# Optimization experiments

Measured on AMD Instinct MI355X. Metric: run time of the kernel, lower is better.

The kernel has to match this reference:

```python
import jax, jax.numpy as jnp
import numpy as np

KSIZE = 3
SOFTMAX_SCALE = 10.0


def extract_patches(x):
    # x: [B, C, H, W] -> patches [B, H*W, C, 3, 3]
    # Matches F.unfold(same_padding(x), kernel=3, stride=1) then
    # reshape(B, C, 3, 3, L).permute(0, 4, 1, 2, 3).
    B, C, H, W = x.shape
    xp = jnp.pad(x, ((0, 0), (0, 0), (1, 1), (1, 1)))
    # p[b, c, i, j, y, x] = xp[b, c, y+i, x+j]
    p = jnp.stack(
        [jnp.stack([xp[:, :, i:i + H, j:j + W] for j in range(KSIZE)], axis=2)
         for i in range(KSIZE)], axis=2)  # [B, C, 3, 3, H, W]
    return p.transpose(0, 4, 5, 1, 2, 3).reshape(B, H * W, C, KSIZE, KSIZE)


def _conv_same(x, w):
    # x: [Cin, H, W], w: [Cout, Cin, 3, 3] -> [Cout, H, W] (pad 1, stride 1)
    return jax.lax.conv_general_dilated(
        x[None], w, window_strides=(1, 1), padding=((1, 1), (1, 1)),
        dimension_numbers=('NCHW', 'OIHW', 'NCHW'))[0]


def setup_inputs() -> dict:
    key = jax.random.key(0)
    kf, kb = jax.random.split(key)
    f = jax.random.normal(kf, (4, 64, 64, 64), dtype=jnp.float32)
    b = jax.random.normal(kb, (4, 64, 64, 64), dtype=jnp.float32)
    return {"f": f, "b": b}


def reference(f, b):
    B, C, Hf, Wf = f.shape
    # Per-sample dynamic kernels from background patches: [B, L, C, 3, 3]
    w = extract_patches(b)
    # Correlation: per-sample conv of f with its own L patch-kernels -> [B, L, Hf, Wf]
    scores = jax.vmap(_conv_same)(f, w)
    # Scaled softmax over the L patch axis
    attn = jax.nn.softmax(scores * SOFTMAX_SCALE, axis=1)
    # conv_transpose2d(attn, w, stride=1, padding=1) == SAME conv with
    # spatially-flipped kernels and in/out channels swapped.
    w_t = jnp.flip(w, axis=(-2, -1)).transpose(0, 2, 1, 3, 4)  # [B, C, L, 3, 3]
    y = jax.vmap(_conv_same)(attn, w_t) / 9.0  # [B, C, Hf, Wf]
    return (y, w.reshape(B, -1, KSIZE, KSIZE))
```

## Files before the change

kernel.cpp:

```cpp
#include <hip/hip_runtime.h>
#include <hip/hip_bf16.h>
#include <hip/hip_fp16.h>
#include <stdint.h>


typedef unsigned short ushort_t;
typedef __attribute__((ext_vector_type(8))) short bf16x8;
typedef __attribute__((ext_vector_type(4))) float f32x4;

#define RSTRIDE  16777216ull
#define ASTRIDE  16777216ull
#define PSTRIDE  33554432ull
#define SSTRIDE  65536ull

__device__ __forceinline__ float bf2f(ushort_t u){
  union { float f; uint32_t i; } v; v.i = ((uint32_t)u) << 16; return v.f;
}
__device__ __forceinline__ ushort_t f2bf(float f){
  union { float f; uint32_t i; } v; v.f = f;
  uint32_t x = v.i;
  return (ushort_t)((x + 0x7fffu + ((x >> 16) & 1u)) >> 16);
}

__global__ __launch_bounds__(256) void k_prep2(const float* __restrict__ bin,
                                               float* __restrict__ wout,
                                               float* __restrict__ yzero){
  __shared__ float ls[2304];
  int tid = threadIdx.x;
  int t = blockIdx.x * 256 + tid;
  yzero[t] = 0.f;
  int c  = t & 63;
  int l  = (t >> 6) & 4095;
  int bb = t >> 18;
  int y = l >> 6, x = l & 63;
  const float* src = bin + (((size_t)(bb * 64 + c)) << 12);
  float* dst = ls + tid * 9;
  #pragma unroll
  for (int i = 0; i < 3; i++){
    int yy = y + i - 1;
    #pragma unroll
    for (int j = 0; j < 3; j++){
      int xx = x + j - 1;
      float v = 0.f;
      if ((unsigned)yy < 64u && (unsigned)xx < 64u) v = src[(yy << 6) + xx];
      dst[i * 3 + j] = v;
    }
  }
  __syncthreads();
  float* wbase = wout + (size_t)blockIdx.x * 2304;
  #pragma unroll
  for (int idx = tid; idx < 576; idx += 256)
    *(float4*)(wbase + (idx << 2)) = *(const float4*)(ls + (idx << 2));
}

__global__ __launch_bounds__(256, 2) void k_rgemm(const float* __restrict__ f,
                                                  const float* __restrict__ bin,
                                                  float* __restrict__ R,
                                                  int bt0){
  __shared__ float As[64][128];
  __shared__ float Bs[64][128];
  int bt = bt0 + blockIdx.z;
  int m0 = blockIdx.x << 7;
  int n0 = blockIdx.y << 7;
  const float* fb = f   + (((size_t)bt) << 18);
  const float* bb = bin + (((size_t)bt) << 18);
  float* Rb = R + (size_t)blockIdx.z * RSTRIDE;
  int t = threadIdx.x;
  for (int idx = t; idx < 64 * 128; idx += 256){
    int c = idx >> 7, m = idx & 127;
    As[c][m] = fb[(c << 12) + m0 + m];
    Bs[c][m] = bb[(c << 12) + n0 + m];
  }
  __syncthreads();
  int tx = t & 15, ty = t >> 4;
  float acc[8][8];
  #pragma unroll
  for (int i = 0; i < 8; i++)
    #pragma unroll
    for (int j = 0; j < 8; j++) acc[i][j] = 0.f;

  for (int c = 0; c < 64; c++){
    float4 a0 = *(const float4*)&As[c][(ty << 3)];
    float4 a1 = *(const float4*)&As[c][(ty << 3) + 4];
    float4 b0 = *(const float4*)&Bs[c][(tx << 2)];
    float4 b1 = *(const float4*)&Bs[c][64 + (tx << 2)];
    float av[8] = {a0.x, a0.y, a0.z, a0.w, a1.x, a1.y, a1.z, a1.w};
    float bv[8] = {b0.x, b0.y, b0.z, b0.w, b1.x, b1.y, b1.z, b1.w};
    #pragma unroll
    for (int i = 0; i < 8; i++)
      #pragma unroll
      for (int j = 0; j < 8; j++) acc[i][j] += av[i] * bv[j];
  }
  #pragma unroll
  for (int i = 0; i < 8; i++){
    float* dst = Rb + ((size_t)(m0 + (ty << 3) + i) << 12) + n0;
    *(float4*)(dst + (tx << 2))      = make_float4(acc[i][0], acc[i][1], acc[i][2], acc[i][3]);
    *(float4*)(dst + 64 + (tx << 2)) = make_float4(acc[i][4], acc[i][5], acc[i][6], acc[i][7]);
  }
}

__global__ __launch_bounds__(256, 2) void k_softmax4(const float* __restrict__ Rg,
                                                     ushort_t* __restrict__ attng,
                                                     __half* __restrict__ scaleg){
  __shared__ float Rt[24][392];
  const int t  = threadIdx.x;
  const int bb = blockIdx.x;
  const float* R = Rg + (size_t)blockIdx.y * RSTRIDE;
  ushort_t* attn = attng + (size_t)blockIdx.y * ASTRIDE;
  __half* scale = scaleg + (size_t)blockIdx.y * SSTRIDE;
  const int inner = bb >> 3;
  const int ty = ((bb & 7) << 1) | (inner & 1);
  const int tx = inner >> 1;
  const int p0 = ty << 2, q0 = tx << 1;
  const int qi = t >> 5, kt = t & 31;
  const int pi = qi >> 1, qj = qi & 1;
  const int ktx = kt & 15;

  float M = -3.0e38f, L = 0.f;
  float mref[16];
  float4 rbuf[10];

  int row = ((p0 + pi) << 6) + q0 + qj;
  ushort_t* arow = attn + ((size_t)row << 12);

  #pragma unroll
  for (int i = 0; i < 10; i++){
    int idx = t + (i << 8);
    float4 v = make_float4(0.f, 0.f, 0.f, 0.f);
    if (idx < 2352){
      unsigned r = (unsigned)idx / 98u;
      int fo = idx - (int)r * 98;
      int rp = p0 - 1 + (int)(r >> 2);
      int rq = q0 - 1 + (int)(r & 3);
      int kg = -68 + (fo << 2);
      if ((unsigned)rp < 64u && (unsigned)rq < 64u && (unsigned)kg <= 4092u)
        v = *(const float4*)(R + (((size_t)((rp << 6) + rq)) << 12) + kg);
    }
    rbuf[i] = v;
  }

  #pragma unroll
  for (int c = 0; c < 16; c++){
    __syncthreads();
    #pragma unroll
    for (int i = 0; i < 10; i++){
      int idx = t + (i << 8);
      if (idx < 2352) ((float4*)&Rt[0][0])[idx] = rbuf[i];
    }
    __syncthreads();
    if (c < 15){
      const int k0 = (c + 1) << 8;
      #pragma unroll
      for (int i = 0; i < 10; i++){
        int idx = t + (i << 8);
        float4 v = make_float4(0.f, 0.f, 0.f, 0.f);
        if (idx < 2352){
          unsigned r = (unsigned)idx / 98u;
          int fo = idx - (int)r * 98;
          int rp = p0 - 1 + (int)(r >> 2);
          int rq = q0 - 1 + (int)(r & 3);
          int kg = k0 - 68 + (fo << 2);
          if ((unsigned)rp < 64u && (unsigned)rq < 64u && (unsigned)kg <= 4092u)
            v = *(const float4*)(R + (((size_t)((rp << 6) + rq)) << 12) + kg);
        }
        rbuf[i] = v;
      }
    }
    float4 sv[2];
    #pragma unroll
    for (int j = 0; j < 2; j++){
      int y = (c << 2) + (j << 1) + (kt >> 4);
      int sa0 = (j << 7) + (kt << 2) + 68;
      float4 s = make_float4(0.f, 0.f, 0.f, 0.f);
      #pragma unroll
      for (int a = -1; a <= 1; a++){
        if ((unsigned)(y + a) < 64u){
          int rb = (pi + 1 + a) << 2;
          int sa = sa0 + (a << 6);
          float4 A0 = *(const float4*)&Rt[rb + qj][sa];
          float4 A1 = *(const float4*)&Rt[rb + qj + 1][sa];
          float4 A2 = *(const float4*)&Rt[rb + qj + 2][sa];
          float Lv = __shfl_up(A0.w, 1);
          float Rv = __shfl_down(A2.x, 1);
          s.x += (ktx == 0 ? 0.f : Lv) + A1.x + A2.y;
          s.y += A0.x + A1.y + A2.z;
          s.z += A0.y + A1.z + A2.w;
          s.w += A0.z + A1.w + (ktx == 15 ? 0.f : Rv);
        }
      }
      s.x *= 10.f; s.y *= 10.f; s.z *= 10.f; s.w *= 10.f;
      sv[j] = s;
    }
    float mc = M;
    #pragma unroll
    for (int j = 0; j < 2; j++)
      mc = fmaxf(mc, fmaxf(fmaxf(sv[j].x, sv[j].y), fmaxf(sv[j].z, sv[j].w)));
    #pragma unroll
    for (int off = 1; off < 32; off <<= 1) mc = fmaxf(mc, __shfl_xor(mc, off));
    float lnew = L * __expf(M - mc);
    #pragma unroll
    for (int j = 0; j < 2; j++){
      float ex = __expf(sv[j].x - mc), ey = __expf(sv[j].y - mc);
      float ez = __expf(sv[j].z - mc), ew = __expf(sv[j].w - mc);
      lnew += ex + ey + ez + ew;
      ushort4 o; o.x = f2bf(ex); o.y = f2bf(ey); o.z = f2bf(ez); o.w = f2bf(ew);
      *(ushort4*)&arow[(c << 8) + (j << 7) + (kt << 2)] = o;
    }
    L = lnew; M = mc; mref[c] = mc;
  }
  #pragma unroll
  for (int off = 1; off < 32; off <<= 1) L += __shfl_xor(L, off);
  if (kt == 0){
    float invL = 1.0f / L;
    __half hs[16];
    #pragma unroll
    for (int c = 0; c < 16; c++) hs[c] = __float2half(__expf(mref[c] - M) * invL);
    *(uint4*)&scale[(row << 4)]     = ((uint4*)hs)[0];
    *(uint4*)&scale[(row << 4) + 8] = ((uint4*)hs)[1];
  }
}

__global__ __launch_bounds__(256, 2) void k_pstencil5(const ushort_t* __restrict__ attng,
                                                      const __half* __restrict__ scaleg,
                                                      ushort_t* __restrict__ Pg){
  __shared__ float At[24][392];
  __shared__ float Sc[24][16];
  const int t  = threadIdx.x;
  const int bb = blockIdx.x;
  const ushort_t* attn = attng + (size_t)blockIdx.y * ASTRIDE;
  const __half* scale = scaleg + (size_t)blockIdx.y * SSTRIDE;
  ushort_t* P = Pg + (size_t)blockIdx.y * PSTRIDE;
  const int inner = bb >> 3;
  const int ty = ((bb & 7) << 1) | (inner & 1);
  const int tx = inner >> 1;
  const int p0 = ty << 2, q0 = tx << 1;
  const int qi = t >> 5, kt = t & 31;
  const int pi = qi >> 1, qj = qi & 1;
  const int ktx = kt & 15;

  int row = ((p0 + pi) << 6) + q0 + qj;
  ushort_t* prow = P + ((size_t)row << 12);
  const float inv9 = 1.0f / 9.0f;

  for (int i = t; i < 384; i += 256){
    int r = i >> 4, cc = i & 15;
    int rp = p0 - 1 + (r >> 2);
    int rq = q0 - 1 + (r & 3);
    float v = 0.f;
    if ((unsigned)rp < 64u && (unsigned)rq < 64u)
      v = __half2float(scale[(((rp << 6) + rq) << 4) + cc]);
    Sc[r][cc] = v;
  }

  uint2 rbuf[10];
  #pragma unroll
  for (int i = 0; i < 10; i++){
    int idx = t + (i << 8);
    uint2 v = make_uint2(0u, 0u);
    if (idx < 2352){
      unsigned r = (unsigned)idx / 98u;
      int fo = idx - (int)r * 98;
      int rp = p0 - 1 + (int)(r >> 2);
      int rq = q0 - 1 + (int)(r & 3);
      int kg = -68 + (fo << 2);
      if ((unsigned)rp < 64u && (unsigned)rq < 64u && (unsigned)kg <= 4092u)
        v = *(const uint2*)(attn + (((size_t)((rp << 6) + rq)) << 12) + kg);
    }
    rbuf[i] = v;
  }

  #pragma unroll
  for (int c = 0; c < 16; c++){
    __syncthreads();
    #pragma unroll
    for (int i = 0; i < 10; i++){
      int idx = t + (i << 8);
      if (idx < 2352){
        unsigned r = (unsigned)idx / 98u;
        int fo = idx - (int)r * 98;
        int key = (c << 8) - 68 + (fo << 2);
        key = key < 0 ? 0 : (key > 4095 ? 4095 : key);
        float sc = Sc[r][key >> 8];
        uint2 u = rbuf[i];
        float4 w;
        { union { uint32_t q; float f; } a_, b_;
          a_.q = u.x << 16; b_.q = u.x & 0xffff0000u; w.x = a_.f * sc; w.y = b_.f * sc; }
        { union { uint32_t q; float f; } a_, b_;
          a_.q = u.y << 16; b_.q = u.y & 0xffff0000u; w.z = a_.f * sc; w.w = b_.f * sc; }
        ((float4*)&At[0][0])[idx] = w;
      }
    }
    __syncthreads();
    if (c < 15){
      const int k0 = (c + 1) << 8;
      #pragma unroll
      for (int i = 0; i < 10; i++){
        int idx = t + (i << 8);
        uint2 v = make_uint2(0u, 0u);
        if (idx < 2352){
          unsigned r = (unsigned)idx / 98u;
          int fo = idx - (int)r * 98;
          int rp = p0 - 1 + (int)(r >> 2);
          int rq = q0 - 1 + (int)(r & 3);
          int kg = k0 - 68 + (fo << 2);
          if ((unsigned)rp < 64u && (unsigned)rq < 64u && (unsigned)kg <= 4092u)
            v = *(const uint2*)(attn + (((size_t)((rp << 6) + rq)) << 12) + kg);
        }
        rbuf[i] = v;
      }
    }
    #pragma unroll
    for (int j = 0; j < 2; j++){
      int y = (c << 2) + (j << 1) + (kt >> 4);
      int sa0 = (j << 7) + (kt << 2) + 68;
      float4 s = make_float4(0.f, 0.f, 0.f, 0.f);
      #pragma unroll
      for (int a = -1; a <= 1; a++){
        if ((unsigned)(y + a) < 64u){
          int rb = (pi + 1 + a) << 2;
          int sa = sa0 + (a << 6);
          float4 A0 = *(const float4*)&At[rb + qj][sa];
          float4 A1 = *(const float4*)&At[rb + qj + 1][sa];
          float4 A2 = *(const float4*)&At[rb + qj + 2][sa];
          float Lv = __shfl_up(A0.w, 1);
          float Rv = __shfl_down(A2.x, 1);
          s.x += (ktx == 0 ? 0.f : Lv) + A1.x + A2.y;
          s.y += A0.x + A1.y + A2.z;
          s.z += A0.y + A1.z + A2.w;
          s.w += A0.z + A1.w + (ktx == 15 ? 0.f : Rv);
        }
      }
      ushort4 o;
      o.x = f2bf(s.x * inv9);
      o.y = f2bf(s.y * inv9);
      o.z = f2bf(s.z * inv9);
      o.w = f2bf(s.w * inv9);
      *(ushort4*)&prow[(c << 8) + (j << 7) + (kt << 2)] = o;
    }
  }
}

__global__ __launch_bounds__(256) void k_ygemm2(const float* __restrict__ bin,
                                                const ushort_t* __restrict__ Pg,
                                                float* __restrict__ y,
                                                int bt0){
  const int t = threadIdx.x;
  const int lane = t & 63, wv = t >> 6;
  const int n = lane & 15, quad = lane >> 4;
  const int bt = bt0 + blockIdx.z;
  const int pq0 = blockIdx.x << 6;
  const int k0  = blockIdx.y << 8;
  const float*    bbase = bin + (((size_t)bt) << 18);
  const ushort_t* Prow  = Pg + (size_t)blockIdx.z * PSTRIDE
                             + (((size_t)(pq0 + (wv << 4) + n)) << 12);

  f32x4 acc[4];
  #pragma unroll
  for (int cb = 0; cb < 4; cb++) acc[cb] = (f32x4){0.f, 0.f, 0.f, 0.f};

  #pragma unroll 2
  for (int kb = k0; kb < k0 + 256; kb += 32){
    int ko = kb + (quad << 3);
    bf16x8 pf = *(const bf16x8*)(Prow + ko);
    #pragma unroll
    for (int cb = 0; cb < 4; cb++){
      const float* bp = bbase + (((cb << 4) + n) << 12) + ko;
      float4 b0 = *(const float4*)bp;
      float4 b1 = *(const float4*)(bp + 4);
      bf16x8 bf;
      bf[0] = (short)f2bf(b0.x); bf[1] = (short)f2bf(b0.y);
      bf[2] = (short)f2bf(b0.z); bf[3] = (short)f2bf(b0.w);
      bf[4] = (short)f2bf(b1.x); bf[5] = (short)f2bf(b1.y);
      bf[6] = (short)f2bf(b1.z); bf[7] = (short)f2bf(b1.w);
      acc[cb] = __builtin_amdgcn_mfma_f32_16x16x32_bf16(bf, pf, acc[cb], 0, 0, 0);
    }
  }
  int pql = pq0 + (wv << 4) + n;
  #pragma unroll
  for (int cb = 0; cb < 4; cb++)
    #pragma unroll
    for (int r = 0; r < 4; r++){
      int c = (cb << 4) + (quad << 2) + r;
      atomicAdd(&y[(((size_t)(bt * 64 + c)) << 12) + pql], acc[cb][r]);
    }
}

extern "C" void kernel_launch(void* const* d_in, const int* in_sizes, int n_in,
                              void* d_out, int out_size, void* d_ws, size_t ws_size,
                              hipStream_t stream){
  const float* f = (const float*)d_in[0];
  const float* b = (const float*)d_in[1];
  float* out  = (float*)d_out;
  float* yout = out;
  float* wout = out + 1048576;

  const size_t RB  = RSTRIDE * 4;
  const size_t AB  = ASTRIDE * 2;
  const size_t SCB = SSTRIDE * 2;
  const size_t PER = RB + AB + SCB;

  int nb = 1;
  if (ws_size >= 4 * PER) nb = 4;
  else if (ws_size >= 2 * PER) nb = 2;

  k_prep2<<<4096, 256, 0, stream>>>(b, wout, yout);

  float*    R     = (float*)d_ws;
  ushort_t* attn  = (ushort_t*)((char*)d_ws + (size_t)nb * RB);
  __half*   scale = (__half*)((char*)d_ws + (size_t)nb * (RB + AB));
  ushort_t* P     = (ushort_t*)d_ws;
  for (int bt0 = 0; bt0 < 4; bt0 += nb){
    k_rgemm    <<<dim3(32, 32, nb), 256, 0, stream>>>(f, b, R, bt0);
    k_softmax4 <<<dim3(512, nb),    256, 0, stream>>>(R, attn, scale);
    k_pstencil5<<<dim3(512, nb),    256, 0, stream>>>(attn, scale, P);
    k_ygemm2   <<<dim3(64, 16, nb), 256, 0, stream>>>(b, P, yout, bt0);
  }
}
```

Baseline: 584.7 us.

## Shrink softmax/stencil tiles to 2x2 rows and replace y atomics with split reduction

```diff
diff --git a/kernel.cpp b/kernel.cpp
--- a/kernel.cpp
+++ b/kernel.cpp
@@ -12,6 +12,7 @@
 #define ASTRIDE  16777216ull
 #define PSTRIDE  33554432ull
 #define SSTRIDE  65536ull
+#define YPSTRIDE 4194304ull
 
 __device__ __forceinline__ float bf2f(ushort_t u){
   union { float f; uint32_t i; } v; v.i = ((uint32_t)u) << 16; return v.f;
@@ -23,12 +24,10 @@
 }
 
 __global__ __launch_bounds__(256) void k_prep2(const float* __restrict__ bin,
-                                               float* __restrict__ wout,
-                                               float* __restrict__ yzero){
+                                               float* __restrict__ wout){
   __shared__ float ls[2304];
   int tid = threadIdx.x;
   int t = blockIdx.x * 256 + tid;
-  yzero[t] = 0.f;
   int c  = t & 63;
   int l  = (t >> 6) & 4095;
   int bb = t >> 18;
@@ -99,35 +98,35 @@
   }
 }
 
-__global__ __launch_bounds__(256, 2) void k_softmax4(const float* __restrict__ Rg,
+__global__ __launch_bounds__(256, 2) void k_softmax5(const float* __restrict__ Rg,
                                                      ushort_t* __restrict__ attng,
                                                      __half* __restrict__ scaleg){
-  __shared__ float Rt[24][392];
+  __shared__ float Rt[16][392];
   const int t  = threadIdx.x;
   const int bb = blockIdx.x;
   const float* R = Rg + (size_t)blockIdx.y * RSTRIDE;
   ushort_t* attn = attng + (size_t)blockIdx.y * ASTRIDE;
   __half* scale = scaleg + (size_t)blockIdx.y * SSTRIDE;
   const int inner = bb >> 3;
-  const int ty = ((bb & 7) << 1) | (inner & 1);
-  const int tx = inner >> 1;
-  const int p0 = ty << 2, q0 = tx << 1;
-  const int qi = t >> 5, kt = t & 31;
+  const int ty = ((bb & 7) << 2) | (inner & 3);
+  const int tx = inner >> 2;
+  const int p0 = ty << 1, q0 = tx << 1;
+  const int qi = t >> 6, kt = t & 63;
   const int pi = qi >> 1, qj = qi & 1;
   const int ktx = kt & 15;
 
   float M = -3.0e38f, L = 0.f;
   float mref[16];
-  float4 rbuf[10];
+  float4 rbuf[7];
 
   int row = ((p0 + pi) << 6) + q0 + qj;
   ushort_t* arow = attn + ((size_t)row << 12);
 
   #pragma unroll
-  for (int i = 0; i < 10; i++){
+  for (int i = 0; i < 7; i++){
     int idx = t + (i << 8);
     float4 v = make_float4(0.f, 0.f, 0.f, 0.f);
-    if (idx < 2352){
+    if (idx < 1568){
       unsigned r = (unsigned)idx / 98u;
       int fo = idx - (int)r * 98;
       int rp = p0 - 1 + (int)(r >> 2);
@@ -143,18 +142,18 @@
   for (int c = 0; c < 16; c++){
     __syncthreads();
     #pragma unroll
-    for (int i = 0; i < 10; i++){
+    for (int i = 0; i < 7; i++){
       int idx = t + (i << 8);
-      if (idx < 2352) ((float4*)&Rt[0][0])[idx] = rbuf[i];
+      if (idx < 1568) ((float4*)&Rt[0][0])[idx] = rbuf[i];
     }
     __syncthreads();
     if (c < 15){
       const int k0 = (c + 1) << 8;
       #pragma unroll
-      for (int i = 0; i < 10; i++){
+      for (int i = 0; i < 7; i++){
         int idx = t + (i << 8);
         float4 v = make_float4(0.f, 0.f, 0.f, 0.f);
-        if (idx < 2352){
+        if (idx < 1568){
           unsigned r = (unsigned)idx / 98u;
           int fo = idx - (int)r * 98;
           int rp = p0 - 1 + (int)(r >> 2);
@@ -166,50 +165,38 @@
         rbuf[i] = v;
       }
     }
-    float4 sv[2];
-    #pragma unroll
-    for (int j = 0; j < 2; j++){
-      int y = (c << 2) + (j << 1) + (kt >> 4);
-      int sa0 = (j << 7) + (kt << 2) + 68;
-      float4 s = make_float4(0.f, 0.f, 0.f, 0.f);
-      #pragma unroll
-      for (int a = -1; a <= 1; a++){
-        if ((unsigned)(y + a) < 64u){
-          int rb = (pi + 1 + a) << 2;
-          int sa = sa0 + (a << 6);
-          float4 A0 = *(const float4*)&Rt[rb + qj][sa];
-          float4 A1 = *(const float4*)&Rt[rb + qj + 1][sa];
-          float4 A2 = *(const float4*)&Rt[rb + qj + 2][sa];
-          float Lv = __shfl_up(A0.w, 1);
-          float Rv = __shfl_down(A2.x, 1);
-          s.x += (ktx == 0 ? 0.f : Lv) + A1.x + A2.y;
-          s.y += A0.x + A1.y + A2.z;
-          s.z += A0.y + A1.z + A2.w;
-          s.w += A0.z + A1.w + (ktx == 15 ? 0.f : Rv);
-        }
+    int y = (c << 2) + (kt >> 4);
+    int sa0 = (kt << 2) + 68;
+    float4 s = make_float4(0.f, 0.f, 0.f, 0.f);
+    #pragma unroll
+    for (int a = -1; a <= 1; a++){
+      if ((unsigned)(y + a) < 64u){
+        int rb = (pi + 1 + a) << 2;
+        int sa = sa0 + (a << 6);
+        float4 A0 = *(const float4*)&Rt[rb + qj][sa];
+        float4 A1 = *(const float4*)&Rt[rb + qj + 1][sa];
+        float4 A2 = *(const float4*)&Rt[rb + qj + 2][sa];
+        float Lv = __shfl_up(A0.w, 1);
+        float Rv = __shfl_down(A2.x, 1);
+        s.x += (ktx == 0 ? 0.f : Lv) + A1.x + A2.y;
+        s.y += A0.x + A1.y + A2.z;
+        s.z += A0.y + A1.z + A2.w;
+        s.w += A0.z + A1.w + (ktx == 15 ? 0.f : Rv);
       }
-      s.x *= 10.f; s.y *= 10.f; s.z *= 10.f; s.w *= 10.f;
-      sv[j] = s;
-    }
-    float mc = M;
-    #pragma unroll
-    for (int j = 0; j < 2; j++)
-      mc = fmaxf(mc, fmaxf(fmaxf(sv[j].x, sv[j].y), fmaxf(sv[j].z, sv[j].w)));
-    #pragma unroll
-    for (int off = 1; off < 32; off <<= 1) mc = fmaxf(mc, __shfl_xor(mc, off));
-    float lnew = L * __expf(M - mc);
-    #pragma unroll
-    for (int j = 0; j < 2; j++){
-      float ex = __expf(sv[j].x - mc), ey = __expf(sv[j].y - mc);
-      float ez = __expf(sv[j].z - mc), ew = __expf(sv[j].w - mc);
-      lnew += ex + ey + ez + ew;
-      ushort4 o; o.x = f2bf(ex); o.y = f2bf(ey); o.z = f2bf(ez); o.w = f2bf(ew);
-      *(ushort4*)&arow[(c << 8) + (j << 7) + (kt << 2)] = o;
-    }
-    L = lnew; M = mc; mref[c] = mc;
-  }
-  #pragma unroll
-  for (int off = 1; off < 32; off <<= 1) L += __shfl_xor(L, off);
+    }
+    s.x *= 10.f; s.y *= 10.f; s.z *= 10.f; s.w *= 10.f;
+    float mc = fmaxf(M, fmaxf(fmaxf(s.x, s.y), fmaxf(s.z, s.w)));
+    #pragma unroll
+    for (int off = 1; off < 64; off <<= 1) mc = fmaxf(mc, __shfl_xor(mc, off));
+    float ex = __expf(s.x - mc), ey = __expf(s.y - mc);
+    float ez = __expf(s.z - mc), ew = __expf(s.w - mc);
+    L = L * __expf(M - mc) + ex + ey + ez + ew;
+    ushort4 o; o.x = f2bf(ex); o.y = f2bf(ey); o.z = f2bf(ez); o.w = f2bf(ew);
+    *(ushort4*)&arow[(c << 8) + (kt << 2)] = o;
+    M = mc; mref[c] = mc;
+  }
+  #pragma unroll
+  for (int off = 1; off < 64; off <<= 1) L += __shfl_xor(L, off);
   if (kt == 0){
     float invL = 1.0f / L;
     __half hs[16];
@@ -220,21 +207,21 @@
   }
 }
 
-__global__ __launch_bounds__(256, 2) void k_pstencil5(const ushort_t* __restrict__ attng,
+__global__ __launch_bounds__(256, 2) void k_pstencil6(const ushort_t* __restrict__ attng,
                                                       const __half* __restrict__ scaleg,
                                                       ushort_t* __restrict__ Pg){
-  __shared__ float At[24][392];
-  __shared__ float Sc[24][16];
+  __shared__ float At[16][392];
+  __shared__ float Sc[16][16];
   const int t  = threadIdx.x;
   const int bb = blockIdx.x;
   const ushort_t* attn = attng + (size_t)blockIdx.y * ASTRIDE;
   const __half* scale = scaleg + (size_t)blockIdx.y * SSTRIDE;
   ushort_t* P = Pg + (size_t)blockIdx.y * PSTRIDE;
   const int inner = bb >> 3;
-  const int ty = ((bb & 7) << 1) | (inner & 1);
-  const int tx = inner >> 1;
-  const int p0 = ty << 2, q0 = tx << 1;
-  const int qi = t >> 5, kt = t & 31;
+  const int ty = ((bb & 7) << 2) | (inner & 3);
+  const int tx = inner >> 2;
+  const int p0 = ty << 1, q0 = tx << 1;
+  const int qi = t >> 6, kt = t & 63;
   const int pi = qi >> 1, qj = qi & 1;
   const int ktx = kt & 15;
 
@@ -242,8 +229,8 @@
   ushort_t* prow = P + ((size_t)row << 12);
   const float inv9 = 1.0f / 9.0f;
 
-  for (int i = t; i < 384; i += 256){
-    int r = i >> 4, cc = i & 15;
+  {
+    int r = t >> 4, cc = t & 15;
     int rp = p0 - 1 + (r >> 2);
     int rq = q0 - 1 + (r & 3);
     float v = 0.f;
@@ -252,12 +239,12 @@
     Sc[r][cc] = v;
   }
 
-  uint2 rbuf[10];
-  #pragma unroll
-  for (int i = 0; i < 10; i++){
+  uint2 rbuf[7];
+  #pragma unroll
+  for (int i = 0; i < 7; i++){
     int idx = t + (i << 8);
     uint2 v = make_uint2(0u, 0u);
-    if (idx < 2352){
+    if (idx < 1568){
       unsigned r = (unsigned)idx / 98u;
       int fo = idx - (int)r * 98;
       int rp = p0 - 1 + (int)(r >> 2);
@@ -273,9 +260,9 @@
   for (int c = 0; c < 16; c++){
     __syncthreads();
     #pragma unroll
-    for (int i = 0; i < 10; i++){
+    for (int i = 0; i < 7; i++){
       int idx = t + (i << 8);
-      if (idx < 2352){
+      if (idx < 1568){
         unsigned r = (unsigned)idx / 98u;
         int fo = idx - (int)r * 98;
         int key = (c << 8) - 68 + (fo << 2);
@@ -294,10 +281,10 @@
     if (c < 15){
       const int k0 = (c + 1) << 8;
       #pragma unroll
-      for (int i = 0; i < 10; i++){
+      for (int i = 0; i < 7; i++){
         int idx = t + (i << 8);
         uint2 v = make_uint2(0u, 0u);
-        if (idx < 2352){
+        if (idx < 1568){
           unsigned r = (unsigned)idx / 98u;
           int fo = idx - (int)r * 98;
           int rp = p0 - 1 + (int)(r >> 2);
@@ -309,50 +296,49 @@
         rbuf[i] = v;
       }
     }
-    #pragma unroll
-    for (int j = 0; j < 2; j++){
-      int y = (c << 2) + (j << 1) + (kt >> 4);
-      int sa0 = (j << 7) + (kt << 2) + 68;
-      float4 s = make_float4(0.f, 0.f, 0.f, 0.f);
-      #pragma unroll
-      for (int a = -1; a <= 1; a++){
-        if ((unsigned)(y + a) < 64u){
-          int rb = (pi + 1 + a) << 2;
-          int sa = sa0 + (a << 6);
-          float4 A0 = *(const float4*)&At[rb + qj][sa];
-          float4 A1 = *(const float4*)&At[rb + qj + 1][sa];
-          float4 A2 = *(const float4*)&At[rb + qj + 2][sa];
-          float Lv = __shfl_up(A0.w, 1);
-          float Rv = __shfl_down(A2.x, 1);
-          s.x += (ktx == 0 ? 0.f : Lv) + A1.x + A2.y;
-          s.y += A0.x + A1.y + A2.z;
-          s.z += A0.y + A1.z + A2.w;
-          s.w += A0.z + A1.w + (ktx == 15 ? 0.f : Rv);
-        }
+    int y = (c << 2) + (kt >> 4);
+    int sa0 = (kt << 2) + 68;
+    float4 s = make_float4(0.f, 0.f, 0.f, 0.f);
+    #pragma unroll
+    for (int a = -1; a <= 1; a++){
+      if ((unsigned)(y + a) < 64u){
+        int rb = (pi + 1 + a) << 2;
+        int sa = sa0 + (a << 6);
+        float4 A0 = *(const float4*)&At[rb + qj][sa];
+        float4 A1 = *(const float4*)&At[rb + qj + 1][sa];
+        float4 A2 = *(const float4*)&At[rb + qj + 2][sa];
+        float Lv = __shfl_up(A0.w, 1);
+        float Rv = __shfl_down(A2.x, 1);
+        s.x += (ktx == 0 ? 0.f : Lv) + A1.x + A2.y;
+        s.y += A0.x + A1.y + A2.z;
+        s.z += A0.y + A1.z + A2.w;
+        s.w += A0.z + A1.w + (ktx == 15 ? 0.f : Rv);
       }
-      ushort4 o;
-      o.x = f2bf(s.x * inv9);
-      o.y = f2bf(s.y * inv9);
-      o.z = f2bf(s.z * inv9);
-      o.w = f2bf(s.w * inv9);
-      *(ushort4*)&prow[(c << 8) + (j << 7) + (kt << 2)] = o;
-    }
-  }
-}
-
-__global__ __launch_bounds__(256) void k_ygemm2(const float* __restrict__ bin,
+    }
+    ushort4 o;
+    o.x = f2bf(s.x * inv9);
+    o.y = f2bf(s.y * inv9);
+    o.z = f2bf(s.z * inv9);
+    o.w = f2bf(s.w * inv9);
+    *(ushort4*)&prow[(c << 8) + (kt << 2)] = o;
+  }
+}
+
+__global__ __launch_bounds__(256) void k_ygemm3(const float* __restrict__ bin,
                                                 const ushort_t* __restrict__ Pg,
-                                                float* __restrict__ y,
+                                                float* __restrict__ ypartg,
                                                 int bt0){
   const int t = threadIdx.x;
   const int lane = t & 63, wv = t >> 6;
   const int n = lane & 15, quad = lane >> 4;
   const int bt = bt0 + blockIdx.z;
   const int pq0 = blockIdx.x << 6;
-  const int k0  = blockIdx.y << 8;
+  const int split = blockIdx.y;
+  const int k0  = split << 8;
   const float*    bbase = bin + (((size_t)bt) << 18);
   const ushort_t* Prow  = Pg + (size_t)blockIdx.z * PSTRIDE
                              + (((size_t)(pq0 + (wv << 4) + n)) << 12);
+  float* ypart = ypartg + (size_t)blockIdx.z * YPSTRIDE;
 
   f32x4 acc[4];
   #pragma unroll
@@ -381,8 +367,19 @@
     #pragma unroll
     for (int r = 0; r < 4; r++){
       int c = (cb << 4) + (quad << 2) + r;
-      atomicAdd(&y[(((size_t)(bt * 64 + c)) << 12) + pql], acc[cb][r]);
-    }
+      ypart[((size_t)((split << 6) + c) << 12) + pql] = acc[cb][r];
+    }
+}
+
+__global__ __launch_bounds__(256) void k_yreduce(const float* __restrict__ ypartg,
+                                                 float* __restrict__ y,
+                                                 int bt0){
+  int e = blockIdx.x * 256 + threadIdx.x;
+  const float* part = ypartg + (size_t)blockIdx.y * YPSTRIDE;
+  float s = 0.f;
+  #pragma unroll
+  for (int k = 0; k < 16; k++) s += part[e + (k << 18)];
+  y[(((size_t)(bt0 + blockIdx.y)) << 18) + e] = s;
 }
 
 extern "C" void kernel_launch(void* const* d_in, const int* in_sizes, int n_in,
@@ -403,16 +400,18 @@
   if (ws_size >= 4 * PER) nb = 4;
   else if (ws_size >= 2 * PER) nb = 2;
 
-  k_prep2<<<4096, 256, 0, stream>>>(b, wout, yout);
+  k_prep2<<<4096, 256, 0, stream>>>(b, wout);
 
   float*    R     = (float*)d_ws;
   ushort_t* attn  = (ushort_t*)((char*)d_ws + (size_t)nb * RB);
   __half*   scale = (__half*)((char*)d_ws + (size_t)nb * (RB + AB));
   ushort_t* P     = (ushort_t*)d_ws;
+  float*    ypart = (float*)attn;
   for (int bt0 = 0; bt0 < 4; bt0 += nb){
-    k_rgemm    <<<dim3(32, 32, nb), 256, 0, stream>>>(f, b, R, bt0);
-    k_softmax4 <<<dim3(512, nb),    256, 0, stream>>>(R, attn, scale);
-    k_pstencil5<<<dim3(512, nb),    256, 0, stream>>>(attn, scale, P);
-    k_ygemm2   <<<dim3(64, 16, nb), 256, 0, stream>>>(b, P, yout, bt0);
-  }
-}
+    k_rgemm    <<<dim3(32, 32, nb),  256, 0, stream>>>(f, b, R, bt0);
+    k_softmax5 <<<dim3(1024, nb),    256, 0, stream>>>(R, attn, scale);
+    k_pstencil6<<<dim3(1024, nb),    256, 0, stream>>>(attn, scale, P);
+    k_ygemm3   <<<dim3(64, 16, nb),  256, 0, stream>>>(b, P, ypart, bt0);
+    k_yreduce  <<<dim3(1024, nb),    256, 0, stream>>>(ypart, yout, bt0);
+  }
+}
```

After: 617.0 us. 1.06x slower.
